# Kernel optimization log

Measured on AMD Instinct MI355X. Metric: run time of the kernel, lower is better.

Reference implementation:

```python
import jax, jax.numpy as jnp
import numpy as np


def _mlp(x, ws, bs):
    # Linear->ReLU between layers, final Linear has no activation
    for i, (w, b) in enumerate(zip(ws, bs)):
        x = x @ w + b
        if i < len(ws) - 1:
            x = jax.nn.relu(x)
    return x


def setup_inputs() -> dict:
    key = jax.random.key(0)
    ks = jax.random.split(key, 24)
    n, q, H, W, dim = 2, 131072, 64, 2048, 64
    num = 4
    depth = jax.random.normal(ks[0], (n, 3, H, W), dtype=jnp.float32)
    feat = jax.random.normal(ks[1], (n, dim, H, W), dtype=jnp.float32)
    coord = jax.random.uniform(ks[2], (n, q, 2), dtype=jnp.float32, minval=-1.0, maxval=1.0)

    def lin(k, din, dout):
        kw, kb = jax.random.split(k)
        s = 1.0 / np.sqrt(din)
        w = jax.random.uniform(kw, (din, dout), minval=-s, maxval=s, dtype=jnp.float32)
        b = jax.random.uniform(kb, (dout,), minval=-s, maxval=s, dtype=jnp.float32)
        return w, b

    # pos_embedd: 2*num=8 -> [dim, num//2*dim] = [64,128] -> num*dim=256
    pe_dims = [2 * num, dim, (num // 2) * dim, num * dim]
    # encoder_xy: num*dim=256 -> [num*dim, num//2*dim, dim] = [256,128,64] -> num=4
    enc_dims = [num * dim, num * dim, (num // 2) * dim, dim, num]
    inp = {"depth": depth, "feat": feat, "coord": coord}
    for i in range(3):
        w, b = lin(ks[3 + i], pe_dims[i], pe_dims[i + 1])
        inp[f"pe_w{i}"] = w
        inp[f"pe_b{i}"] = b
    for i in range(4):
        w, b = lin(ks[8 + i], enc_dims[i], enc_dims[i + 1])
        inp[f"enc_w{i}"] = w
        inp[f"enc_b{i}"] = b
    return inp


def reference(depth, feat, coord,
              pe_w0, pe_b0, pe_w1, pe_b1, pe_w2, pe_b2,
              enc_w0, enc_b0, enc_w1, enc_b1, enc_w2, enc_b2, enc_w3, enc_b3):
    n, C, H, W = feat.shape
    q = coord.shape[1]
    eps = 1e-6
    # xy range-view magnitude map [n, H, W]
    xy = jnp.sqrt(depth[:, 1] ** 2 + depth[:, 2] ** 2)

    rx = 1.0 / H  # 2 / H / 2
    ry = 1.0 / W
    # offsets in the same (vx outer, vy inner) order as the torch loop
    offs = jnp.array([[-1.0, -1.0], [-1.0, 1.0], [1.0, -1.0], [1.0, 1.0]], dtype=coord.dtype)
    shift = offs * jnp.array([rx, ry], dtype=coord.dtype) + eps  # [4,2]
    c = jnp.clip(coord[None] + shift[:, None, None, :], -1.0 + 1e-6, 1.0 - 1e-6)  # [4,n,q,2]

    # nearest grid_sample, align_corners=False: unnormalized = ((g+1)*size - 1)/2, then round
    iy = jnp.clip(jnp.round(((c[..., 0] + 1.0) * H - 1.0) * 0.5).astype(jnp.int32), 0, H - 1)
    ix = jnp.clip(jnp.round(((c[..., 1] + 1.0) * W - 1.0) * 0.5).astype(jnp.int32), 0, W - 1)

    b = jnp.arange(n)[None, :, None]  # broadcasts against [4,n,q]
    q_feat = feat[b, :, iy, ix]      # [4,n,q,C] nearest-gathered features
    pred_xy = xy[b, iy, ix]          # [4,n,q]

    # sampled pixel-center coords (what grid_sample of feat_coord returns)
    qc_y = -1.0 + (2.0 * iy.astype(coord.dtype) + 1.0) / H
    qc_x = -1.0 + (2.0 * ix.astype(coord.dtype) + 1.0) / W
    rel = jnp.stack([(coord[None, ..., 0] - qc_y) * H,
                     (coord[None, ..., 1] - qc_x) * W], axis=-1)  # [4,n,q,2]

    # rearrange 't n q d -> (n q) (t d)'
    qf = q_feat.transpose(1, 2, 0, 3).reshape(n * q, 4 * C)
    rc = rel.transpose(1, 2, 0, 3).reshape(n * q, 4 * 2)

    qf = qf + _mlp(rc, [pe_w0, pe_w1, pe_w2], [pe_b0, pe_b1, pe_b2])
    logits = _mlp(qf, [enc_w0, enc_w1, enc_w2, enc_w3], [enc_b0, enc_b1, enc_b2, enc_b3])  # [nq,4]
    w = jax.nn.softmax(logits, axis=1)

    p = pred_xy.transpose(1, 2, 0).reshape(n * q, 4)  # 't n q -> (n q) t'
    ret = jnp.sum(p * w, axis=1).reshape(n, q, 1)     # [nq,1,4] @ [nq,4,1]
    return ret
```

## Files before the change

### kernel.cpp

```cpp
#include <hip/hip_runtime.h>
#include <hip/hip_runtime_api.h>
#include <math.h>

#define NBATCH 2
#define QQ     131072
#define HH     64
#define WWID   2048
#define CC     64
#define HWSZ   (HH*WWID)

constexpr int ROWS    = 64;
constexpr int THREADS = 512;

constexpr int ASTR_B = 512;

constexpr int OFF_A   = 0;
constexpr int OFF_TAP = 32768;
constexpr int OFF_PXY = OFF_TAP + 1024;
constexpr int OFF_E3  = OFF_PXY + 1024;
constexpr int LDS_BYTES = OFF_E3 + 1024;

constexpr int WOFF_PE0 = 0;
constexpr int WOFF_PE1 = 4096;
constexpr int WOFF_PE2 = 12288;
constexpr int WOFF_E0  = 45056;
constexpr int WOFF_E1  = 110592;
constexpr int WOFF_E2  = 143360;
constexpr int WTOTAL   = 151552;

typedef __attribute__((ext_vector_type(8))) short bf16x8;
typedef __attribute__((ext_vector_type(4))) float f32x4;

__device__ __forceinline__ ushort f2bf(float f) {
    union { float f; unsigned u; } x; x.f = f;
    unsigned r = x.u + 0x7fffu + ((x.u >> 16) & 1u);
    return (ushort)(r >> 16);
}
__device__ __forceinline__ float bf2f(ushort h) {
    union { unsigned u; float f; } x; x.u = ((unsigned)h) << 16;
    return x.f;
}
__device__ __forceinline__ unsigned cvtpk(float a, float b) {
    unsigned r;
    asm("v_cvt_pk_bf16_f32 %0, %1, %2" : "=v"(r) : "v"(a), "v"(b));
    return r;
}

__device__ __forceinline__ int swA(int row, int colByte) {
    return row * ASTR_B + (colByte ^ ((row & 7) << 4));
}

struct WDesc { const float* src; int K; int N; int kshift; };
struct WPack { WDesc d[6]; };

__global__ __launch_bounds__(256) void prep_weights(WPack p, ushort* __restrict__ dst)
{
    int e = blockIdx.x * 256 + threadIdx.x;
    int off = 0;
    #pragma unroll
    for (int L = 0; L < 6; ++L) {
        const int Kp = 1 << p.d[L].kshift;
        const int N  = p.d[L].N;
        const int sz = N * Kp;
        if (e < sz) {
            const int n = e / Kp;
            const int k = e & (Kp - 1);
            const float v = (k < p.d[L].K) ? p.d[L].src[(size_t)k * N + n] : 0.f;
            const int chunk = k >> 6;
            const int kk    = (k >> 5) & 1;
            const int tile  = chunk * ((N >> 4) * 2) + (n >> 4) * 2 + kk;
            const int lane  = (n & 15) + (((k >> 3) & 3) << 4);
            const int j     = k & 7;
            dst[off + tile * 512 + lane * 8 + j] = f2bf(v);
            return;
        }
        e -= sz; off += sz;
    }
}

__global__ __launch_bounds__(256) void prep_feat(
    const float* __restrict__ depth, const float* __restrict__ feat,
    ushort* __restrict__ nhwc, float* __restrict__ xy)
{
    const int idx = blockIdx.x * 256 + threadIdx.x;
    const int b   = idx >> 17;
    const int yx  = idx & (HWSZ - 1);

    const float d1 = depth[(b * 3 + 1) * HWSZ + yx];
    const float d2 = depth[(b * 3 + 2) * HWSZ + yx];
    xy[idx] = sqrtf(d1 * d1 + d2 * d2);

    const float* fp = feat + (size_t)b * CC * HWSZ + yx;
    ushort* op = nhwc + (size_t)idx * CC;
    #pragma unroll
    for (int c = 0; c < CC; c += 8) {
        union { uint4 v; ushort u[8]; } t;
        #pragma unroll
        for (int j = 0; j < 8; ++j) t.u[j] = f2bf(fp[(size_t)(c + j) * HWSZ]);
        *(uint4*)(op + c) = t.v;
    }
}

template <int K, int N, bool RELU>
__device__ __forceinline__ void dense_layer(
    char* __restrict__ sA, const ushort* __restrict__ Wt,
    const float* __restrict__ Bg, int tid)
{
    constexpr int TN  = N / 64;
    constexpr int NCH = K / 64;

    const int lane = tid & 63, wv = tid >> 6;
    const int wm = wv >> 2, wn = wv & 3;
    const int row0 = wm * 32;
    const int col0 = wn * (N / 4);
    const int lrow = lane & 15;
    const int lkb  = (lane >> 4) * 16;

    f32x4 acc[2][TN];
    #pragma unroll
    for (int tm = 0; tm < 2; ++tm)
        #pragma unroll
        for (int tn = 0; tn < TN; ++tn) acc[tm][tn] = (f32x4){0.f, 0.f, 0.f, 0.f};

    const char* wbase = (const char*)Wt + (size_t)lane * 16;

    for (int c = 0; c < NCH; ++c) {
        #pragma unroll
        for (int ks = 0; ks < 64; ks += 32) {
            const int cb = (c * 64 + ks) * 2 + lkb;
            const bf16x8 a0 = *(const bf16x8*)(sA + swA(row0 +      lrow, cb));
            const bf16x8 a1 = *(const bf16x8*)(sA + swA(row0 + 16 + lrow, cb));
            #pragma unroll
            for (int tn = 0; tn < TN; ++tn) {
                const int tile = c * ((N >> 4) * 2) + ((col0 >> 4) + tn) * 2 + (ks >> 5);
                const bf16x8 bw = *(const bf16x8*)(wbase + tile * 1024);
                acc[0][tn] = __builtin_amdgcn_mfma_f32_16x16x32_bf16(bw, a0, acc[0][tn], 0, 0, 0);
                acc[1][tn] = __builtin_amdgcn_mfma_f32_16x16x32_bf16(bw, a1, acc[1][tn], 0, 0, 0);
            }
        }
    }
    __syncthreads();

    #pragma unroll
    for (int tn = 0; tn < TN; ++tn) {
        const int colb = col0 + tn * 16 + (lane >> 4) * 4;
        const float4 b4 = *(const float4*)(Bg + colb);
        #pragma unroll
        for (int tm = 0; tm < 2; ++tm) {
            float v0 = acc[tm][tn][0] + b4.x;
            float v1 = acc[tm][tn][1] + b4.y;
            float v2 = acc[tm][tn][2] + b4.z;
            float v3 = acc[tm][tn][3] + b4.w;
            if (RELU) {
                v0 = fmaxf(v0, 0.f); v1 = fmaxf(v1, 0.f);
                v2 = fmaxf(v2, 0.f); v3 = fmaxf(v3, 0.f);
            }
            uint2 pk;
            pk.x = cvtpk(v0, v1);
            pk.y = cvtpk(v2, v3);
            const int row = row0 + tm * 16 + lrow;
            *(uint2*)(sA + swA(row, colb * 2)) = pk;
        }
    }
    __syncthreads();
}

template <bool USE_WS>
__global__ __launch_bounds__(512, 4) void fused_kernel(
    const float* __restrict__ depth, const float* __restrict__ feat,
    const float* __restrict__ coord,
    const float* __restrict__ pb0, const float* __restrict__ pb1,
    const float* __restrict__ pb2,
    const float* __restrict__ eb0, const float* __restrict__ eb1,
    const float* __restrict__ eb2,
    const float* __restrict__ ew3, const float* __restrict__ eb3,
    const ushort* __restrict__ wt,
    const ushort* __restrict__ nhwc, const float* __restrict__ xyws,
    float* __restrict__ out)
{
    extern __shared__ char lds[];
    char*  sA   = lds + OFF_A;
    int*   sTap = (int*)(lds + OFF_TAP);
    float* sPxy = (float*)(lds + OFF_PXY);
    float* sE3  = (float*)(lds + OFF_E3);

    const int tid  = threadIdx.x;
    const int row0g = blockIdx.x * ROWS;
    const int b     = row0g >> 17;

    if (tid < 256) sE3[tid] = ew3[tid];

    {
        const int r = tid >> 3, c16 = tid & 7;
        uint4 z; z.x = z.y = z.z = z.w = 0u;
        *(uint4*)(sA + r * ASTR_B + c16 * 16) = z;
    }
    __syncthreads();

    if (tid < 256) {
        #pragma clang fp contract(off)
        const int r = tid >> 2, s = tid & 3;
        const int row = row0g + r;
        const float cy = coord[row * 2 + 0];
        const float cx = coord[row * 2 + 1];
        const float offy = (s < 2) ? -1.f : 1.f;
        const float offx = (s & 1) ? 1.f : -1.f;
        const float rx = 1.f / (float)HH, ry = 1.f / (float)WWID;
        float ccy = cy + (offy * rx + 1e-6f);
        float ccx = cx + (offx * ry + 1e-6f);
        ccy = fminf(fmaxf(ccy, -1.f + 1e-6f), 1.f - 1e-6f);
        ccx = fminf(fmaxf(ccx, -1.f + 1e-6f), 1.f - 1e-6f);
        int iy = (int)rintf(((ccy + 1.f) * (float)HH - 1.f) * 0.5f);
        int ix = (int)rintf(((ccx + 1.f) * (float)WWID - 1.f) * 0.5f);
        iy = min(max(iy, 0), HH - 1);
        ix = min(max(ix, 0), WWID - 1);
        const float qcy = -1.f + (2.f * (float)iy + 1.f) / (float)HH;
        const float qcx = -1.f + (2.f * (float)ix + 1.f) / (float)WWID;
        *(ushort*)(sA + swA(r, s * 4 + 0)) = f2bf((cy - qcy) * (float)HH);
        *(ushort*)(sA + swA(r, s * 4 + 2)) = f2bf((cx - qcx) * (float)WWID);
        const int tap = iy * WWID + ix;
        sTap[r * 4 + s] = tap;
        float px;
        if (USE_WS) {
            px = xyws[b * HWSZ + tap];
        } else {
            const float d1 = depth[(b * 3 + 1) * HWSZ + tap];
            const float d2 = depth[(b * 3 + 2) * HWSZ + tap];
            px = sqrtf(d1 * d1 + d2 * d2);
        }
        sPxy[r * 4 + s] = px;
    }
    __syncthreads();

    dense_layer<64,  64,  true >(sA, wt + WOFF_PE0, pb0, tid);
    dense_layer<64,  128, true >(sA, wt + WOFF_PE1, pb1, tid);
    dense_layer<128, 256, false>(sA, wt + WOFF_PE2, pb2, tid);

    {
        const int r = tid >> 3, h = tid & 7;
        const int s = h >> 1, half = h & 1;
        const int tap = sTap[r * 4 + s];
        const int cb0 = s * 128 + half * 64;
        if (USE_WS) {
            const ushort* src = nhwc + ((size_t)b * HWSZ + tap) * CC + half * 32;
            #pragma unroll
            for (int g = 0; g < 4; ++g) {
                char* dp = sA + swA(r, cb0 + g * 16);
                union { uint4 v; ushort u[8]; } a, d;
                a.v = *(const uint4*)(src + g * 8);
                d.v = *(uint4*)dp;
                float s0 = bf2f(a.u[0]) + bf2f(d.u[0]);
                float s1 = bf2f(a.u[1]) + bf2f(d.u[1]);
                float s2 = bf2f(a.u[2]) + bf2f(d.u[2]);
                float s3 = bf2f(a.u[3]) + bf2f(d.u[3]);
                float s4 = bf2f(a.u[4]) + bf2f(d.u[4]);
                float s5 = bf2f(a.u[5]) + bf2f(d.u[5]);
                float s6 = bf2f(a.u[6]) + bf2f(d.u[6]);
                float s7 = bf2f(a.u[7]) + bf2f(d.u[7]);
                uint4 o;
                o.x = cvtpk(s0, s1); o.y = cvtpk(s2, s3);
                o.z = cvtpk(s4, s5); o.w = cvtpk(s6, s7);
                *(uint4*)dp = o;
            }
        } else {
            const float* fp = feat + (size_t)b * CC * HWSZ + tap;
            #pragma unroll 8
            for (int c = 0; c < 32; ++c) {
                const int ch = half * 32 + c;
                ushort* p = (ushort*)(sA + swA(r, cb0 + c * 2));
                *p = f2bf(bf2f(*p) + fp[(size_t)ch * HWSZ]);
            }
        }
    }
    __syncthreads();

    dense_layer<256, 256, true>(sA, wt + WOFF_E0, eb0, tid);
    dense_layer<256, 128, true>(sA, wt + WOFF_E1, eb1, tid);
    dense_layer<128, 64,  true>(sA, wt + WOFF_E2, eb2, tid);

    if (tid < 256) {
        const int r = tid >> 2, sub = tid & 3;
        float l0 = 0.f, l1 = 0.f, l2 = 0.f, l3 = 0.f;
        #pragma unroll
        for (int kk = 0; kk < 16; ++kk) {
            const int k = sub * 16 + kk;
            const float a = bf2f(*(const ushort*)(sA + swA(r, k * 2)));
            const float4 w = ((const float4*)sE3)[k];
            l0 = fmaf(a, w.x, l0);
            l1 = fmaf(a, w.y, l1);
            l2 = fmaf(a, w.z, l2);
            l3 = fmaf(a, w.w, l3);
        }
        #pragma unroll
        for (int m = 1; m <= 2; m <<= 1) {
            l0 += __shfl_xor(l0, m);
            l1 += __shfl_xor(l1, m);
            l2 += __shfl_xor(l2, m);
            l3 += __shfl_xor(l3, m);
        }
        if (sub == 0) {
            l0 += eb3[0]; l1 += eb3[1]; l2 += eb3[2]; l3 += eb3[3];
            const float m  = fmaxf(fmaxf(l0, l1), fmaxf(l2, l3));
            const float e0 = expf(l0 - m), e1 = expf(l1 - m);
            const float e2 = expf(l2 - m), e3 = expf(l3 - m);
            const float inv = 1.f / (e0 + e1 + e2 + e3);
            const float o = (sPxy[r * 4 + 0] * e0 + sPxy[r * 4 + 1] * e1 +
                             sPxy[r * 4 + 2] * e2 + sPxy[r * 4 + 3] * e3) * inv;
            out[row0g + r] = o;
        }
    }
}

extern "C" void kernel_launch(void* const* d_in, const int* in_sizes, int n_in,
                              void* d_out, int out_size, void* d_ws, size_t ws_size,
                              hipStream_t stream)
{
    const float* depth = (const float*)d_in[0];
    const float* feat  = (const float*)d_in[1];
    const float* coord = (const float*)d_in[2];
    const float* pw0 = (const float*)d_in[3],  *pb0 = (const float*)d_in[4];
    const float* pw1 = (const float*)d_in[5],  *pb1 = (const float*)d_in[6];
    const float* pw2 = (const float*)d_in[7],  *pb2 = (const float*)d_in[8];
    const float* ew0 = (const float*)d_in[9],  *eb0 = (const float*)d_in[10];
    const float* ew1 = (const float*)d_in[11], *eb1 = (const float*)d_in[12];
    const float* ew2 = (const float*)d_in[13], *eb2 = (const float*)d_in[14];
    const float* ew3 = (const float*)d_in[15], *eb3 = (const float*)d_in[16];
    float* out = (float*)d_out;

    const size_t nhwc_bytes = (size_t)NBATCH * HWSZ * CC * 2;
    const size_t xy_bytes   = (size_t)NBATCH * HWSZ * 4;
    const size_t wt_bytes   = (size_t)WTOTAL * 2;
    const bool use_ws = (ws_size >= nhwc_bytes + xy_bytes + wt_bytes);

    ushort* nhwc = (ushort*)d_ws;
    float*  xyws = (float*)((char*)d_ws + nhwc_bytes);
    ushort* wt   = use_ws ? (ushort*)((char*)d_ws + nhwc_bytes + xy_bytes)
                          : (ushort*)d_ws;

    WPack pack;
    pack.d[0] = { pw0, 8,   64,  6 };
    pack.d[1] = { pw1, 64,  128, 6 };
    pack.d[2] = { pw2, 128, 256, 7 };
    pack.d[3] = { ew0, 256, 256, 8 };
    pack.d[4] = { ew1, 256, 128, 8 };
    pack.d[5] = { ew2, 128, 64,  7 };
    prep_weights<<<WTOTAL / 256, 256, 0, stream>>>(pack, wt);

    const int nblocks = (NBATCH * QQ) / ROWS;

    if (use_ws) {
        prep_feat<<<(NBATCH * HWSZ) / 256, 256, 0, stream>>>(depth, feat, nhwc, xyws);
        fused_kernel<true><<<nblocks, THREADS, LDS_BYTES, stream>>>(
            depth, feat, coord, pb0, pb1, pb2, eb0, eb1, eb2, ew3, eb3,
            wt, nhwc, xyws, out);
    } else {
        fused_kernel<false><<<nblocks, THREADS, LDS_BYTES, stream>>>(
            depth, feat, coord, pb0, pb1, pb2, eb0, eb1, eb2, ew3, eb3,
            wt, nhwc, xyws, out);
    }
}
```

Before: 156.4 us.

## Ping-pong LDS activation buffers and compute first PE layer in scalar fp32

Activations now alternate between two LDS buffers, so each dense layer reads one buffer and writes the other. This drops the barrier that separated the MFMA reads from the epilogue writes. The tiny K=8 first positional-embedding layer is computed directly in fp32 on the VALU from shuffled relative coordinates, replacing a zero-padded K=64 MFMA layer, and the LDS zero-fill pass is removed. In exchange, LDS per block roughly doubles to about 68KB. That likely cuts resident blocks per CU below the 4 the launch bounds request, which lowers occupancy and latency hiding for the gathers.

After: 175.2 us. +12.0%, slower.

```diff
diff --git a/kernel.cpp b/kernel.cpp
--- a/kernel.cpp
+++ b/kernel.cpp
@@ -14,8 +14,9 @@
 
 constexpr int ASTR_B = 512;
 
-constexpr int OFF_A   = 0;
-constexpr int OFF_TAP = 32768;
+constexpr int OFF_A0  = 0;
+constexpr int OFF_A1  = 32768;
+constexpr int OFF_TAP = 65536;
 constexpr int OFF_PXY = OFF_TAP + 1024;
 constexpr int OFF_E3  = OFF_PXY + 1024;
 constexpr int LDS_BYTES = OFF_E3 + 1024;
@@ -103,7 +104,7 @@
 
 template <int K, int N, bool RELU>
 __device__ __forceinline__ void dense_layer(
-    char* __restrict__ sA, const ushort* __restrict__ Wt,
+    const char* src, char* dst, const ushort* __restrict__ Wt,
     const float* __restrict__ Bg, int tid)
 {
     constexpr int TN  = N / 64;
@@ -128,8 +129,8 @@
         #pragma unroll
         for (int ks = 0; ks < 64; ks += 32) {
             const int cb = (c * 64 + ks) * 2 + lkb;
-            const bf16x8 a0 = *(const bf16x8*)(sA + swA(row0 +      lrow, cb));
-            const bf16x8 a1 = *(const bf16x8*)(sA + swA(row0 + 16 + lrow, cb));
+            const bf16x8 a0 = *(const bf16x8*)(src + swA(row0 +      lrow, cb));
+            const bf16x8 a1 = *(const bf16x8*)(src + swA(row0 + 16 + lrow, cb));
             #pragma unroll
             for (int tn = 0; tn < TN; ++tn) {
                 const int tile = c * ((N >> 4) * 2) + ((col0 >> 4) + tn) * 2 + (ks >> 5);
@@ -139,7 +140,6 @@
             }
         }
     }
-    __syncthreads();
 
     #pragma unroll
     for (int tn = 0; tn < TN; ++tn) {
@@ -159,7 +159,7 @@
             pk.x = cvtpk(v0, v1);
             pk.y = cvtpk(v2, v3);
             const int row = row0 + tm * 16 + lrow;
-            *(uint2*)(sA + swA(row, colb * 2)) = pk;
+            *(uint2*)(dst + swA(row, colb * 2)) = pk;
         }
     }
     __syncthreads();
@@ -169,8 +169,8 @@
 __global__ __launch_bounds__(512, 4) void fused_kernel(
     const float* __restrict__ depth, const float* __restrict__ feat,
     const float* __restrict__ coord,
-    const float* __restrict__ pb0, const float* __restrict__ pb1,
-    const float* __restrict__ pb2,
+    const float* __restrict__ pw0, const float* __restrict__ pb0,
+    const float* __restrict__ pb1, const float* __restrict__ pb2,
     const float* __restrict__ eb0, const float* __restrict__ eb1,
     const float* __restrict__ eb2,
     const float* __restrict__ ew3, const float* __restrict__ eb3,
@@ -179,73 +179,114 @@
     float* __restrict__ out)
 {
     extern __shared__ char lds[];
-    char*  sA   = lds + OFF_A;
+    char*  sA0  = lds + OFF_A0;
+    char*  sA1  = lds + OFF_A1;
     int*   sTap = (int*)(lds + OFF_TAP);
     float* sPxy = (float*)(lds + OFF_PXY);
     float* sE3  = (float*)(lds + OFF_E3);
 
     const int tid  = threadIdx.x;
+    const int lane = tid & 63;
     const int row0g = blockIdx.x * ROWS;
     const int b     = row0g >> 17;
 
-    if (tid < 256) sE3[tid] = ew3[tid];
+    if (tid >= 256 && tid < 512 && (tid - 256) < 256) sE3[tid - 256] = ew3[tid - 256];
+
+    if (tid < 256) {
+        const int r = tid >> 2, s = tid & 3;
+        float rely, relx;
+        {
+            #pragma clang fp contract(off)
+            const int row = row0g + r;
+            const float cy = coord[row * 2 + 0];
+            const float cx = coord[row * 2 + 1];
+            const float offy = (s < 2) ? -1.f : 1.f;
+            const float offx = (s & 1) ? 1.f : -1.f;
+            const float rx = 1.f / (float)HH, ry = 1.f / (float)WWID;
+            float ccy = cy + (offy * rx + 1e-6f);
+            float ccx = cx + (offx * ry + 1e-6f);
+            ccy = fminf(fmaxf(ccy, -1.f + 1e-6f), 1.f - 1e-6f);
+            ccx = fminf(fmaxf(ccx, -1.f + 1e-6f), 1.f - 1e-6f);
+            int iy = (int)rintf(((ccy + 1.f) * (float)HH - 1.f) * 0.5f);
+            int ix = (int)rintf(((ccx + 1.f) * (float)WWID - 1.f) * 0.5f);
+            iy = min(max(iy, 0), HH - 1);
+            ix = min(max(ix, 0), WWID - 1);
+            const float qcy = -1.f + (2.f * (float)iy + 1.f) / (float)HH;
+            const float qcx = -1.f + (2.f * (float)ix + 1.f) / (float)WWID;
+            rely = (cy - qcy) * (float)HH;
+            relx = (cx - qcx) * (float)WWID;
+            const int tap = iy * WWID + ix;
+            sTap[r * 4 + s] = tap;
+            float px;
+            if (USE_WS) {
+                px = xyws[b * HWSZ + tap];
+            } else {
+                const float d1 = depth[(b * 3 + 1) * HWSZ + tap];
+                const float d2 = depth[(b * 3 + 2) * HWSZ + tap];
+                px = sqrtf(d1 * d1 + d2 * d2);
+            }
+            sPxy[r * 4 + s] = px;
+        }
+
+        const int qb = lane & ~3;
+        float rc[8];
+        #pragma unroll
+        for (int j = 0; j < 4; ++j) {
+            rc[j * 2 + 0] = __shfl(rely, qb + j);
+            rc[j * 2 + 1] = __shfl(relx, qb + j);
+        }
+        const int c0 = s * 16;
+        float4 o0 = *(const float4*)(pb0 + c0);
+        float4 o1 = *(const float4*)(pb0 + c0 + 4);
+        float4 o2 = *(const float4*)(pb0 + c0 + 8);
+        float4 o3 = *(const float4*)(pb0 + c0 + 12);
+        #pragma unroll
+        for (int k = 0; k < 8; ++k) {
+            const float a = rc[k];
+            const float4 w0 = *(const float4*)(pw0 + k * 64 + c0);
+            const float4 w1 = *(const float4*)(pw0 + k * 64 + c0 + 4);
+            const float4 w2 = *(const float4*)(pw0 + k * 64 + c0 + 8);
+            const float4 w3 = *(const float4*)(pw0 + k * 64 + c0 + 12);
+            o0.x = fmaf(a, w0.x, o0.x); o0.y = fmaf(a, w0.y, o0.y);
+            o0.z = fmaf(a, w0.z, o0.z); o0.w = fmaf(a, w0.w, o0.w);
+            o1.x = fmaf(a, w1.x, o1.x); o1.y = fmaf(a, w1.y, o1.y);
+            o1.z = fmaf(a, w1.z, o1.z); o1.w = fmaf(a, w1.w, o1.w);
+            o2.x = fmaf(a, w2.x, o2.x); o2.y = fmaf(a, w2.y, o2.y);
+            o2.z = fmaf(a, w2.z, o2.z); o2.w = fmaf(a, w2.w, o2.w);
+            o3.x = fmaf(a, w3.x, o3.x); o3.y = fmaf(a, w3.y, o3.y);
+            o3.z = fmaf(a, w3.z, o3.z); o3.w = fmaf(a, w3.w, o3.w);
+        }
+        o0.x = fmaxf(o0.x, 0.f); o0.y = fmaxf(o0.y, 0.f);
+        o0.z = fmaxf(o0.z, 0.f); o0.w = fmaxf(o0.w, 0.f);
+        o1.x = fmaxf(o1.x, 0.f); o1.y = fmaxf(o1.y, 0.f);
+        o1.z = fmaxf(o1.z, 0.f); o1.w = fmaxf(o1.w, 0.f);
+        o2.x = fmaxf(o2.x, 0.f); o2.y = fmaxf(o2.y, 0.f);
+        o2.z = fmaxf(o2.z, 0.f); o2.w = fmaxf(o2.w, 0.f);
+        o3.x = fmaxf(o3.x, 0.f); o3.y = fmaxf(o3.y, 0.f);
+        o3.z = fmaxf(o3.z, 0.f); o3.w = fmaxf(o3.w, 0.f);
+        uint4 lo, hi;
+        lo.x = cvtpk(o0.x, o0.y); lo.y = cvtpk(o0.z, o0.w);
+        lo.z = cvtpk(o1.x, o1.y); lo.w = cvtpk(o1.z, o1.w);
+        hi.x = cvtpk(o2.x, o2.y); hi.y = cvtpk(o2.z, o2.w);
+        hi.z = cvtpk(o3.x, o3.y); hi.w = cvtpk(o3.z, o3.w);
+        *(uint4*)(sA0 + swA(r, s * 32))      = lo;
+        *(uint4*)(sA0 + swA(r, s * 32 + 16)) = hi;
+    }
+    __syncthreads();
+
+    dense_layer<64,  128, true >(sA0, sA1, wt + WOFF_PE1, pb1, tid);
+    dense_layer<128, 256, false>(sA1, sA0, wt + WOFF_PE2, pb2, tid);
 
     {
-        const int r = tid >> 3, c16 = tid & 7;
-        uint4 z; z.x = z.y = z.z = z.w = 0u;
-        *(uint4*)(sA + r * ASTR_B + c16 * 16) = z;
-    }
-    __syncthreads();
-
-    if (tid < 256) {
-        #pragma clang fp contract(off)
-        const int r = tid >> 2, s = tid & 3;
-        const int row = row0g + r;
-        const float cy = coord[row * 2 + 0];
-        const float cx = coord[row * 2 + 1];
-        const float offy = (s < 2) ? -1.f : 1.f;
-        const float offx = (s & 1) ? 1.f : -1.f;
-        const float rx = 1.f / (float)HH, ry = 1.f / (float)WWID;
-        float ccy = cy + (offy * rx + 1e-6f);
-        float ccx = cx + (offx * ry + 1e-6f);
-        ccy = fminf(fmaxf(ccy, -1.f + 1e-6f), 1.f - 1e-6f);
-        ccx = fminf(fmaxf(ccx, -1.f + 1e-6f), 1.f - 1e-6f);
-        int iy = (int)rintf(((ccy + 1.f) * (float)HH - 1.f) * 0.5f);
-        int ix = (int)rintf(((ccx + 1.f) * (float)WWID - 1.f) * 0.5f);
-        iy = min(max(iy, 0), HH - 1);
-        ix = min(max(ix, 0), WWID - 1);
-        const float qcy = -1.f + (2.f * (float)iy + 1.f) / (float)HH;
-        const float qcx = -1.f + (2.f * (float)ix + 1.f) / (float)WWID;
-        *(ushort*)(sA + swA(r, s * 4 + 0)) = f2bf((cy - qcy) * (float)HH);
-        *(ushort*)(sA + swA(r, s * 4 + 2)) = f2bf((cx - qcx) * (float)WWID);
-        const int tap = iy * WWID + ix;
-        sTap[r * 4 + s] = tap;
-        float px;
-        if (USE_WS) {
-            px = xyws[b * HWSZ + tap];
-        } else {
-            const float d1 = depth[(b * 3 + 1) * HWSZ + tap];
-            const float d2 = depth[(b * 3 + 2) * HWSZ + tap];
-            px = sqrtf(d1 * d1 + d2 * d2);
-        }
-        sPxy[r * 4 + s] = px;
-    }
-    __syncthreads();
-
-    dense_layer<64,  64,  true >(sA, wt + WOFF_PE0, pb0, tid);
-    dense_layer<64,  128, true >(sA, wt + WOFF_PE1, pb1, tid);
-    dense_layer<128, 256, false>(sA, wt + WOFF_PE2, pb2, tid);
-
-    {
-        const int r = tid >> 3, h = tid & 7;
-        const int s = h >> 1, half = h & 1;
-        const int tap = sTap[r * 4 + s];
-        const int cb0 = s * 128 + half * 64;
+        const int gr = tid >> 3, h = tid & 7;
+        const int gs = h >> 1, half = h & 1;
+        const int tap = sTap[gr * 4 + gs];
+        const int cb0 = gs * 128 + half * 64;
         if (USE_WS) {
             const ushort* src = nhwc + ((size_t)b * HWSZ + tap) * CC + half * 32;
             #pragma unroll
             for (int g = 0; g < 4; ++g) {
-                char* dp = sA + swA(r, cb0 + g * 16);
+                char* dp = sA0 + swA(gr, cb0 + g * 16);
                 union { uint4 v; ushort u[8]; } a, d;
                 a.v = *(const uint4*)(src + g * 8);
                 d.v = *(uint4*)dp;
@@ -267,24 +308,24 @@
             #pragma unroll 8
             for (int c = 0; c < 32; ++c) {
                 const int ch = half * 32 + c;
-                ushort* p = (ushort*)(sA + swA(r, cb0 + c * 2));
+                ushort* p = (ushort*)(sA0 + swA(gr, cb0 + c * 2));
                 *p = f2bf(bf2f(*p) + fp[(size_t)ch * HWSZ]);
             }
         }
     }
     __syncthreads();
 
-    dense_layer<256, 256, true>(sA, wt + WOFF_E0, eb0, tid);
-    dense_layer<256, 128, true>(sA, wt + WOFF_E1, eb1, tid);
-    dense_layer<128, 64,  true>(sA, wt + WOFF_E2, eb2, tid);
+    dense_layer<256, 256, true>(sA0, sA1, wt + WOFF_E0, eb0, tid);
+    dense_layer<256, 128, true>(sA1, sA0, wt + WOFF_E1, eb1, tid);
+    dense_layer<128, 64,  true>(sA0, sA1, wt + WOFF_E2, eb2, tid);
 
     if (tid < 256) {
-        const int r = tid >> 2, sub = tid & 3;
+        const int fr = tid >> 2, sub = tid & 3;
         float l0 = 0.f, l1 = 0.f, l2 = 0.f, l3 = 0.f;
         #pragma unroll
         for (int kk = 0; kk < 16; ++kk) {
             const int k = sub * 16 + kk;
-            const float a = bf2f(*(const ushort*)(sA + swA(r, k * 2)));
+            const float a = bf2f(*(const ushort*)(sA1 + swA(fr, k * 2)));
             const float4 w = ((const float4*)sE3)[k];
             l0 = fmaf(a, w.x, l0);
             l1 = fmaf(a, w.y, l1);
@@ -304,9 +345,9 @@
             const float e0 = expf(l0 - m), e1 = expf(l1 - m);
             const float e2 = expf(l2 - m), e3 = expf(l3 - m);
             const float inv = 1.f / (e0 + e1 + e2 + e3);
-            const float o = (sPxy[r * 4 + 0] * e0 + sPxy[r * 4 + 1] * e1 +
-                             sPxy[r * 4 + 2] * e2 + sPxy[r * 4 + 3] * e3) * inv;
-            out[row0g + r] = o;
+            const float o = (sPxy[fr * 4 + 0] * e0 + sPxy[fr * 4 + 1] * e1 +
+                             sPxy[fr * 4 + 2] * e2 + sPxy[fr * 4 + 3] * e3) * inv;
+            out[row0g + fr] = o;
         }
     }
 }
@@ -350,12 +391,16 @@
 
     if (use_ws) {
         prep_feat<<<(NBATCH * HWSZ) / 256, 256, 0, stream>>>(depth, feat, nhwc, xyws);
+        hipFuncSetAttribute((const void*)fused_kernel<true>,
+                            hipFuncAttributeMaxDynamicSharedMemorySize, LDS_BYTES);
         fused_kernel<true><<<nblocks, THREADS, LDS_BYTES, stream>>>(
-            depth, feat, coord, pb0, pb1, pb2, eb0, eb1, eb2, ew3, eb3,
+            depth, feat, coord, pw0, pb0, pb1, pb2, eb0, eb1, eb2, ew3, eb3,
             wt, nhwc, xyws, out);
     } else {
+        hipFuncSetAttribute((const void*)fused_kernel<false>,
+                            hipFuncAttributeMaxDynamicSharedMemorySize, LDS_BYTES);
         fused_kernel<false><<<nblocks, THREADS, LDS_BYTES, stream>>>(
-            depth, feat, coord, pb0, pb1, pb2, eb0, eb1, eb2, ew3, eb3,
+            depth, feat, coord, pw0, pb0, pb1, pb2, eb0, eb1, eb2, ew3, eb3,
             wt, nhwc, xyws, out);
     }
 }
```
